# Optimization experiments

Hardware: AMD Instinct MI355X
Metric: run time of the kernel (lower is better)

The kernel has to match this reference:

```python
import jax, jax.numpy as jnp
import numpy as np

N_HEADS = 8
NUM_TIME_STEPS = 17  # T = NUM_TIME_STEPS - 1 = 16
MASK_PAD = np.float32(-2**32 + 1)


def setup_inputs() -> dict:
    key = jax.random.key(0)
    ks = jax.random.split(key, 5)
    B, T, D = 32768, NUM_TIME_STEPS - 1, 128
    return {
        "inputs": jax.random.normal(ks[0], (B, T, D), dtype=jnp.float32),
        "pos_emb": jax.random.normal(ks[1], (NUM_TIME_STEPS, D), dtype=jnp.float32) * 0.1,
        "Wq": jax.random.normal(ks[2], (D, D), dtype=jnp.float32) * (1.0 / np.sqrt(D)),
        "Wk": jax.random.normal(ks[3], (D, D), dtype=jnp.float32) * (1.0 / np.sqrt(D)),
        "Wv": jax.random.normal(ks[4], (D, D), dtype=jnp.float32) * (1.0 / np.sqrt(D)),
    }


def reference(inputs, pos_emb, Wq, Wk, Wv):
    B, T, D = inputs.shape
    h = N_HEADS
    dh = Wq.shape[1] // h
    # add positional embeddings for the first T time steps
    x = inputs + pos_emb[:T][None, :, :]  # [B, T, D]
    # QKV projections, then split into heads (torch.split dim=2 + cat dim=0 == head-major [h, B, T, dh])
    def proj(W):
        return jnp.einsum("btd,de->bte", x, W).reshape(B, T, h, dh).transpose(2, 0, 1, 3)
    q, k, v = proj(Wq), proj(Wk), proj(Wv)  # each [h, B, T, dh]
    # scaled scores; NOTE: original scales by sqrt(num_time_steps), not sqrt(head_dim)
    scores = jnp.einsum("hbtd,hbsd->hbts", q, k) / jnp.float32(NUM_TIME_STEPS) ** 0.5
    # causal mask: masked positions set to -2**32+1 (finite pad, as in the original)
    causal = jnp.tril(jnp.ones((T, T), dtype=bool))
    scores = jnp.where(causal[None, None, :, :], scores, MASK_PAD)
    attn = jax.nn.softmax(scores, axis=-1)  # [h, B, T, T]
    o = jnp.einsum("hbts,hbsd->hbtd", attn, v)  # [h, B, T, dh]
    # re-concat heads along feature dim (split dim0 + cat dim2)
    o = o.transpose(1, 2, 0, 3).reshape(B, T, h * dh)
    # feedforward: relu(x) + x
    o = jax.nn.relu(o) + o
    # residual=True: concat with temporal (position-added) inputs along features
    return jnp.concatenate([o, x], axis=2)  # [B, T, output_dim + input_dim]
```

## Files before the change

kernel.cpp:

```cpp
#include <hip/hip_runtime.h>

typedef float    f32x4 __attribute__((ext_vector_type(4)));
typedef __bf16   bf16x8 __attribute__((ext_vector_type(8)));
typedef _Float16 f16x4 __attribute__((ext_vector_type(4)));

typedef __attribute__((address_space(1))) const void gas_void;
typedef __attribute__((address_space(3))) void las_void;

static __device__ __forceinline__ unsigned short f2bf(float f) {
  union { float f; unsigned int u; } a; a.f = f;
  unsigned int r = (a.u + 0x7FFFu + ((a.u >> 16) & 1u)) >> 16;
  return (unsigned short)r;
}

#define QSCALE_L2E 0.34992146f

__global__ void prep_weights(const float* __restrict__ Wq, const float* __restrict__ Wk,
                             const float* __restrict__ Wv, unsigned short* __restrict__ wf) {
  int idx = blockIdx.x * 256 + threadIdx.x;
  if (idx >= 3 * 8 * 4 * 64 * 8) return;
  int i  = idx & 7;
  int p  = (idx >> 3) & 63;
  int kk = (idx >> 9) & 3;
  int n  = (idx >> 11) & 7;
  int w  = idx >> 14;
  const float* W = (w == 0) ? Wq : ((w == 1) ? Wk : Wv);
  float val = W[(kk * 32 + (p >> 4) * 8 + i) * 128 + n * 16 + (p & 15)];
  if (w == 0) val *= QSCALE_L2E;
  wf[idx] = f2bf(val);
}

__global__ void prep_posw(const float* __restrict__ pos, const float* __restrict__ Wq,
                          const float* __restrict__ Wk, const float* __restrict__ Wv,
                          float* __restrict__ pw) {
  int idx = blockIdx.x * 256 + threadIdx.x;
  if (idx >= 3 * 8 * 64 * 4) return;
  int r = idx & 3;
  int l = (idx >> 2) & 63;
  int h = (idx >> 8) & 7;
  int w = idx >> 11;
  const float* W = (w == 0) ? Wq : ((w == 1) ? Wk : Wv);
  int t, d;
  if (w < 2) { t = l & 15;            d = h * 16 + (l >> 4) * 4 + r; }
  else       { t = (l >> 4) * 4 + r;  d = h * 16 + (l & 15); }
  float s = 0.f;
  for (int k = 0; k < 128; ++k) s += pos[t * 128 + k] * W[k * 128 + d];
  if (w == 0) s *= QSCALE_L2E;
  pw[idx] = s;
}

__global__ void __launch_bounds__(256, 2)
attn_main(const float* __restrict__ xin, const float* __restrict__ pos,
          const unsigned short* __restrict__ wfrag, const float* __restrict__ pw,
          float* __restrict__ out, int B) {
  __shared__ __align__(16) float lx[2][2048];

  const int tid   = threadIdx.x;
  const int wid   = tid >> 6;
  const int l     = tid & 63;
  const int frow  = l & 15;
  const int fkq   = l >> 4;
  const int trow0 = fkq * 4;
  const int n0    = wid * 2;

  bf16x8 wf[3][2][4];
#pragma unroll
  for (int w = 0; w < 3; ++w)
#pragma unroll
    for (int hl = 0; hl < 2; ++hl)
#pragma unroll
      for (int kk = 0; kk < 4; ++kk)
        wf[w][hl][kk] = *(const bf16x8*)(wfrag + ((w * 32 + (n0 + hl) * 4 + kk) * 512) + l * 8);

  f32x4 posw[3][2];
#pragma unroll
  for (int w = 0; w < 3; ++w)
#pragma unroll
    for (int hl = 0; hl < 2; ++hl)
      posw[w][hl] = *(const f32x4*)(pw + ((w * 8 + n0 + hl) * 64 + l) * 4);

  const int ptc = wid * 32 + fkq * 8;
  const f32x4 pp0 = *(const f32x4*)(pos + frow * 128 + ptc);
  const f32x4 pp1 = *(const f32x4*)(pos + frow * 128 + ptc + 4);

  const f32x4 zero4 = {0.f, 0.f, 0.f, 0.f};

  const int gsrc0 = frow * 128 + wid * 32 + fkq * 8;

  {
    const float* xb = xin + (size_t)blockIdx.x * 2048;
    __builtin_amdgcn_global_load_lds((gas_void*)(xb + gsrc0),
                                     (las_void*)&lx[0][(wid * 2 + 0) * 256], 16, 0, 0);
    __builtin_amdgcn_global_load_lds((gas_void*)(xb + gsrc0 + 4),
                                     (las_void*)&lx[0][(wid * 2 + 1) * 256], 16, 0, 0);
  }
  int buf = 0;
  const int b0i = blockIdx.x;

  for (int b = b0i; b < B; b += gridDim.x) {
    if (b == b0i) {
      __syncthreads();
    } else {
      asm volatile("s_waitcnt vmcnt(4)" ::: "memory");
      __builtin_amdgcn_s_barrier();
    }

    if (b + (int)gridDim.x < B) {
      const float* xb2 = xin + (size_t)(b + gridDim.x) * 2048;
      __builtin_amdgcn_global_load_lds((gas_void*)(xb2 + gsrc0),
                                       (las_void*)&lx[buf ^ 1][(wid * 2 + 0) * 256], 16, 0, 0);
      __builtin_amdgcn_global_load_lds((gas_void*)(xb2 + gsrc0 + 4),
                                       (las_void*)&lx[buf ^ 1][(wid * 2 + 1) * 256], 16, 0, 0);
    }

    float* ob = out + (size_t)b * 4096;
    const float* lb = &lx[buf][0];

    bf16x8 xf[4];
#pragma unroll
    for (int kk = 0; kk < 4; ++kk) {
      f32x4 a0 = *(const f32x4*)(lb + (2 * kk + 0) * 256 + l * 4);
      f32x4 a1 = *(const f32x4*)(lb + (2 * kk + 1) * 256 + l * 4);
      xf[kk][0] = (__bf16)a0.x; xf[kk][1] = (__bf16)a0.y;
      xf[kk][2] = (__bf16)a0.z; xf[kk][3] = (__bf16)a0.w;
      xf[kk][4] = (__bf16)a1.x; xf[kk][5] = (__bf16)a1.y;
      xf[kk][6] = (__bf16)a1.z; xf[kk][7] = (__bf16)a1.w;
    }
    {
      f32x4 c0 = *(const f32x4*)(lb + (2 * wid + 0) * 256 + l * 4);
      f32x4 c1 = *(const f32x4*)(lb + (2 * wid + 1) * 256 + l * 4);
      *(f32x4*)(ob + frow * 256 + 128 + ptc)     = c0 + pp0;
      *(f32x4*)(ob + frow * 256 + 128 + ptc + 4) = c1 + pp1;
    }

#pragma unroll
    for (int hl = 0; hl < 2; ++hl) {
      f32x4 qa = posw[0][hl], ka = posw[1][hl], va = posw[2][hl];
#pragma unroll
      for (int kk = 0; kk < 4; ++kk) {
        qa = __builtin_amdgcn_mfma_f32_16x16x32_bf16(wf[0][hl][kk], xf[kk], qa, 0, 0, 0);
        ka = __builtin_amdgcn_mfma_f32_16x16x32_bf16(wf[1][hl][kk], xf[kk], ka, 0, 0, 0);
        va = __builtin_amdgcn_mfma_f32_16x16x32_bf16(xf[kk], wf[2][hl][kk], va, 0, 0, 0);
      }
      f16x4 qh, kh, vh;
#pragma unroll
      for (int r = 0; r < 4; ++r) {
        qh[r] = (_Float16)qa[r];
        kh[r] = (_Float16)ka[r];
        vh[r] = (_Float16)va[r];
      }

      f32x4 st = __builtin_amdgcn_mfma_f32_16x16x16f16(kh, qh, zero4, 0, 0, 0);
      float p0 = (trow0 + 0 <= frow) ? __builtin_amdgcn_exp2f(st[0]) : 0.f;
      float p1 = (trow0 + 1 <= frow) ? __builtin_amdgcn_exp2f(st[1]) : 0.f;
      float p2 = (trow0 + 2 <= frow) ? __builtin_amdgcn_exp2f(st[2]) : 0.f;
      float p3 = (trow0 + 3 <= frow) ? __builtin_amdgcn_exp2f(st[3]) : 0.f;
      float ssum = (p0 + p1) + (p2 + p3);
      ssum += __shfl_xor(ssum, 16);
      ssum += __shfl_xor(ssum, 32);
      float inv = __builtin_amdgcn_rcpf(ssum);
      f16x4 ah;
      ah[0] = (_Float16)(p0 * inv);
      ah[1] = (_Float16)(p1 * inv);
      ah[2] = (_Float16)(p2 * inv);
      ah[3] = (_Float16)(p3 * inv);

      f32x4 ot = __builtin_amdgcn_mfma_f32_16x16x16f16(vh, ah, zero4, 0, 0, 0);
      f32x4 ov;
#pragma unroll
      for (int r = 0; r < 4; ++r) {
        float x = ot[r];
        ov[r] = x > 0.f ? 2.f * x : x;
      }
      *(f32x4*)(ob + frow * 256 + (n0 + hl) * 16 + trow0) = ov;
    }

    buf ^= 1;
  }
}

extern "C" void kernel_launch(void* const* d_in, const int* in_sizes, int n_in,
                              void* d_out, int out_size, void* d_ws, size_t ws_size,
                              hipStream_t stream) {
  (void)n_in; (void)out_size; (void)ws_size;
  const float* xin = (const float*)d_in[0];
  const float* pos = (const float*)d_in[1];
  const float* Wq  = (const float*)d_in[2];
  const float* Wk  = (const float*)d_in[3];
  const float* Wv  = (const float*)d_in[4];
  float* out = (float*)d_out;
  unsigned short* wf = (unsigned short*)d_ws;
  float* pw = (float*)((char*)d_ws + 3 * 8 * 4 * 64 * 8 * sizeof(unsigned short));
  int B = in_sizes[0] / 2048;

  hipLaunchKernelGGL(prep_weights, dim3(192), dim3(256), 0, stream, Wq, Wk, Wv, wf);
  hipLaunchKernelGGL(prep_posw, dim3(24), dim3(256), 0, stream, pos, Wq, Wk, Wv, pw);
  hipLaunchKernelGGL(attn_main, dim3(2048), dim3(256), 0, stream, xin, pos, wf, pw, out, B);
}
```

Measured before the change: 177.7 us.

## Process four batch elements per block iteration with larger LDS prefetch

Each block now stages four batch elements per loop iteration, with each wave issuing eight async global-to-LDS loads for one element, and the grid shrinks to 512 blocks. This is meant to increase bytes in flight per prefetch and amortize barriers and loop overhead over more work. It raises LDS use to 64 KB per block and assumes B divides evenly by four times the grid size, dropping the tail handling.

```diff
diff --git a/kernel.cpp b/kernel.cpp
--- a/kernel.cpp
+++ b/kernel.cpp
@@ -53,7 +53,7 @@
 attn_main(const float* __restrict__ xin, const float* __restrict__ pos,
           const unsigned short* __restrict__ wfrag, const float* __restrict__ pw,
           float* __restrict__ out, int B) {
-  __shared__ __align__(16) float lx[2][2048];
+  __shared__ __align__(16) float lx[2][4][2048];
 
   const int tid   = threadIdx.x;
   const int wid   = tid >> 6;
@@ -85,94 +85,101 @@
 
   const f32x4 zero4 = {0.f, 0.f, 0.f, 0.f};
 
-  const int gsrc0 = frow * 128 + wid * 32 + fkq * 8;
+  const int bpi   = gridDim.x * 4;
+  const int niter = B / bpi;
+  const int gsb   = frow * 128 + fkq * 8;
 
   {
-    const float* xb = xin + (size_t)blockIdx.x * 2048;
-    __builtin_amdgcn_global_load_lds((gas_void*)(xb + gsrc0),
-                                     (las_void*)&lx[0][(wid * 2 + 0) * 256], 16, 0, 0);
-    __builtin_amdgcn_global_load_lds((gas_void*)(xb + gsrc0 + 4),
-                                     (las_void*)&lx[0][(wid * 2 + 1) * 256], 16, 0, 0);
+    const float* xb = xin + (size_t)(blockIdx.x * 4 + wid) * 2048;
+#pragma unroll
+    for (int c = 0; c < 8; ++c)
+      __builtin_amdgcn_global_load_lds((gas_void*)(xb + gsb + (c >> 1) * 32 + (c & 1) * 4),
+                                       (las_void*)&lx[0][wid][c * 256], 16, 0, 0);
   }
   int buf = 0;
-  const int b0i = blockIdx.x;
-
-  for (int b = b0i; b < B; b += gridDim.x) {
-    if (b == b0i) {
+
+  for (int it = 0; it < niter; ++it) {
+    const int b0 = blockIdx.x * 4 + it * bpi;
+
+    if (it == 0) {
       __syncthreads();
     } else {
-      asm volatile("s_waitcnt vmcnt(4)" ::: "memory");
+      asm volatile("s_waitcnt vmcnt(16)" ::: "memory");
       __builtin_amdgcn_s_barrier();
     }
 
-    if (b + (int)gridDim.x < B) {
-      const float* xb2 = xin + (size_t)(b + gridDim.x) * 2048;
-      __builtin_amdgcn_global_load_lds((gas_void*)(xb2 + gsrc0),
-                                       (las_void*)&lx[buf ^ 1][(wid * 2 + 0) * 256], 16, 0, 0);
-      __builtin_amdgcn_global_load_lds((gas_void*)(xb2 + gsrc0 + 4),
-                                       (las_void*)&lx[buf ^ 1][(wid * 2 + 1) * 256], 16, 0, 0);
+    if (it + 1 < niter) {
+      const float* xb2 = xin + (size_t)(b0 + bpi + wid) * 2048;
+#pragma unroll
+      for (int c = 0; c < 8; ++c)
+        __builtin_amdgcn_global_load_lds((gas_void*)(xb2 + gsb + (c >> 1) * 32 + (c & 1) * 4),
+                                         (las_void*)&lx[buf ^ 1][wid][c * 256], 16, 0, 0);
     }
-
-    float* ob = out + (size_t)b * 4096;
-    const float* lb = &lx[buf][0];
-
-    bf16x8 xf[4];
-#pragma unroll
-    for (int kk = 0; kk < 4; ++kk) {
-      f32x4 a0 = *(const f32x4*)(lb + (2 * kk + 0) * 256 + l * 4);
-      f32x4 a1 = *(const f32x4*)(lb + (2 * kk + 1) * 256 + l * 4);
-      xf[kk][0] = (__bf16)a0.x; xf[kk][1] = (__bf16)a0.y;
-      xf[kk][2] = (__bf16)a0.z; xf[kk][3] = (__bf16)a0.w;
-      xf[kk][4] = (__bf16)a1.x; xf[kk][5] = (__bf16)a1.y;
-      xf[kk][6] = (__bf16)a1.z; xf[kk][7] = (__bf16)a1.w;
-    }
-    {
-      f32x4 c0 = *(const f32x4*)(lb + (2 * wid + 0) * 256 + l * 4);
-      f32x4 c1 = *(const f32x4*)(lb + (2 * wid + 1) * 256 + l * 4);
-      *(f32x4*)(ob + frow * 256 + 128 + ptc)     = c0 + pp0;
-      *(f32x4*)(ob + frow * 256 + 128 + ptc + 4) = c1 + pp1;
-    }
-
-#pragma unroll
-    for (int hl = 0; hl < 2; ++hl) {
-      f32x4 qa = posw[0][hl], ka = posw[1][hl], va = posw[2][hl];
+    asm volatile("" ::: "memory");
+
+#pragma unroll
+    for (int g = 0; g < 4; ++g) {
+      const float* lb = &lx[buf][g][0];
+      float* ob = out + (size_t)(b0 + g) * 4096;
+
+      bf16x8 xf[4];
 #pragma unroll
       for (int kk = 0; kk < 4; ++kk) {
-        qa = __builtin_amdgcn_mfma_f32_16x16x32_bf16(wf[0][hl][kk], xf[kk], qa, 0, 0, 0);
-        ka = __builtin_amdgcn_mfma_f32_16x16x32_bf16(wf[1][hl][kk], xf[kk], ka, 0, 0, 0);
-        va = __builtin_amdgcn_mfma_f32_16x16x32_bf16(xf[kk], wf[2][hl][kk], va, 0, 0, 0);
+        f32x4 a0 = *(const f32x4*)(lb + (2 * kk + 0) * 256 + l * 4);
+        f32x4 a1 = *(const f32x4*)(lb + (2 * kk + 1) * 256 + l * 4);
+        xf[kk][0] = (__bf16)a0.x; xf[kk][1] = (__bf16)a0.y;
+        xf[kk][2] = (__bf16)a0.z; xf[kk][3] = (__bf16)a0.w;
+        xf[kk][4] = (__bf16)a1.x; xf[kk][5] = (__bf16)a1.y;
+        xf[kk][6] = (__bf16)a1.z; xf[kk][7] = (__bf16)a1.w;
       }
-      f16x4 qh, kh, vh;
-#pragma unroll
-      for (int r = 0; r < 4; ++r) {
-        qh[r] = (_Float16)qa[r];
-        kh[r] = (_Float16)ka[r];
-        vh[r] = (_Float16)va[r];
+      {
+        f32x4 c0 = *(const f32x4*)(lb + (2 * wid + 0) * 256 + l * 4);
+        f32x4 c1 = *(const f32x4*)(lb + (2 * wid + 1) * 256 + l * 4);
+        *(f32x4*)(ob + frow * 256 + 128 + ptc)     = c0 + pp0;
+        *(f32x4*)(ob + frow * 256 + 128 + ptc + 4) = c1 + pp1;
       }
 
-      f32x4 st = __builtin_amdgcn_mfma_f32_16x16x16f16(kh, qh, zero4, 0, 0, 0);
-      float p0 = (trow0 + 0 <= frow) ? __builtin_amdgcn_exp2f(st[0]) : 0.f;
-      float p1 = (trow0 + 1 <= frow) ? __builtin_amdgcn_exp2f(st[1]) : 0.f;
-      float p2 = (trow0 + 2 <= frow) ? __builtin_amdgcn_exp2f(st[2]) : 0.f;
-      float p3 = (trow0 + 3 <= frow) ? __builtin_amdgcn_exp2f(st[3]) : 0.f;
-      float ssum = (p0 + p1) + (p2 + p3);
-      ssum += __shfl_xor(ssum, 16);
-      ssum += __shfl_xor(ssum, 32);
-      float inv = __builtin_amdgcn_rcpf(ssum);
-      f16x4 ah;
-      ah[0] = (_Float16)(p0 * inv);
-      ah[1] = (_Float16)(p1 * inv);
-      ah[2] = (_Float16)(p2 * inv);
-      ah[3] = (_Float16)(p3 * inv);
-
-      f32x4 ot = __builtin_amdgcn_mfma_f32_16x16x16f16(vh, ah, zero4, 0, 0, 0);
-      f32x4 ov;
-#pragma unroll
-      for (int r = 0; r < 4; ++r) {
-        float x = ot[r];
-        ov[r] = x > 0.f ? 2.f * x : x;
+#pragma unroll
+      for (int hl = 0; hl < 2; ++hl) {
+        f32x4 qa = posw[0][hl], ka = posw[1][hl], va = posw[2][hl];
+#pragma unroll
+        for (int kk = 0; kk < 4; ++kk) {
+          qa = __builtin_amdgcn_mfma_f32_16x16x32_bf16(wf[0][hl][kk], xf[kk], qa, 0, 0, 0);
+          ka = __builtin_amdgcn_mfma_f32_16x16x32_bf16(wf[1][hl][kk], xf[kk], ka, 0, 0, 0);
+          va = __builtin_amdgcn_mfma_f32_16x16x32_bf16(xf[kk], wf[2][hl][kk], va, 0, 0, 0);
+        }
+        f16x4 qh, kh, vh;
+#pragma unroll
+        for (int r = 0; r < 4; ++r) {
+          qh[r] = (_Float16)qa[r];
+          kh[r] = (_Float16)ka[r];
+          vh[r] = (_Float16)va[r];
+        }
+
+        f32x4 st = __builtin_amdgcn_mfma_f32_16x16x16f16(kh, qh, zero4, 0, 0, 0);
+        float p0 = (trow0 + 0 <= frow) ? __builtin_amdgcn_exp2f(st[0]) : 0.f;
+        float p1 = (trow0 + 1 <= frow) ? __builtin_amdgcn_exp2f(st[1]) : 0.f;
+        float p2 = (trow0 + 2 <= frow) ? __builtin_amdgcn_exp2f(st[2]) : 0.f;
+        float p3 = (trow0 + 3 <= frow) ? __builtin_amdgcn_exp2f(st[3]) : 0.f;
+        float ssum = (p0 + p1) + (p2 + p3);
+        ssum += __shfl_xor(ssum, 16);
+        ssum += __shfl_xor(ssum, 32);
+        float inv = __builtin_amdgcn_rcpf(ssum);
+        f16x4 ah;
+        ah[0] = (_Float16)(p0 * inv);
+        ah[1] = (_Float16)(p1 * inv);
+        ah[2] = (_Float16)(p2 * inv);
+        ah[3] = (_Float16)(p3 * inv);
+
+        f32x4 ot = __builtin_amdgcn_mfma_f32_16x16x16f16(vh, ah, zero4, 0, 0, 0);
+        f32x4 ov;
+#pragma unroll
+        for (int r = 0; r < 4; ++r) {
+          float x = ot[r];
+          ov[r] = x > 0.f ? 2.f * x : x;
+        }
+        *(f32x4*)(ob + frow * 256 + (n0 + hl) * 16 + trow0) = ov;
       }
-      *(f32x4*)(ob + frow * 256 + (n0 + hl) * 16 + trow0) = ov;
     }
 
     buf ^= 1;
@@ -195,5 +202,5 @@
 
   hipLaunchKernelGGL(prep_weights, dim3(192), dim3(256), 0, stream, Wq, Wk, Wv, wf);
   hipLaunchKernelGGL(prep_posw, dim3(24), dim3(256), 0, stream, pos, Wq, Wk, Wv, pw);
-  hipLaunchKernelGGL(attn_main, dim3(2048), dim3(256), 0, stream, xin, pos, wf, pw, out, B);
-}
+  hipLaunchKernelGGL(attn_main, dim3(512), dim3(256), 0, stream, xin, pos, wf, pw, out, B);
+}
```

After: 173.0 us. 2.6% less time.
